# Kernel optimization log

Hardware: AMD Instinct MI355X
Metric: run time of the kernel (lower is better)

## Reference

```python
import jax, jax.numpy as jnp
import numpy as np

NUM_ATOMS = 1024
NUM_FEATS = 80      # c
NUM_IRREPS = 48     # (l_max+1)^2 * 3 with l_max=3
K3, K2, K1 = 1270, 24, 3  # CG-basis param counts per correlation order


def setup_inputs() -> dict:
    key = jax.random.key(0)
    ks = jax.random.split(key, 7)
    return {
        "node_feats": jax.random.normal(ks[0], (NUM_ATOMS, NUM_FEATS, NUM_IRREPS), jnp.float32),
        "U3": jax.random.normal(ks[1], (NUM_IRREPS, NUM_IRREPS, NUM_IRREPS, K3), jnp.float32),
        "U2": jax.random.normal(ks[2], (NUM_IRREPS, NUM_IRREPS, K2), jnp.float32),
        "U1": jax.random.normal(ks[3], (NUM_IRREPS, K1), jnp.float32),
        "W3": jax.random.normal(ks[4], (K3, NUM_FEATS), jnp.float32),
        "W2": jax.random.normal(ks[5], (K2, NUM_FEATS), jnp.float32),
        "W1": jax.random.normal(ks[6], (K1, NUM_FEATS), jnp.float32),
    }


def reference(node_feats, U3, U2, U1, W3, W2, W1):
    # equation_main: '...ik,kc,bci -> bc...' with U3 [p,q,i,k]
    # -> out [n, c, p, q]
    out = jnp.einsum('pqik,kc,nci->ncpq', U3, W3, node_feats)

    # corr = 2: c_tensor = einsum('...k,kc->c...', U2, W2) -> [c, p, q]
    c2 = jnp.einsum('pqk,kc->cpq', U2, W2) + out          # [n, c, p, q]
    # equation_contract: 'bc...i,bci->bc...'
    out = jnp.einsum('ncpi,nci->ncp', c2, node_feats)     # [n, c, p]

    # corr = 1: c_tensor = einsum('...k,kc->c...', U1, W1) -> [c, p]
    c1 = jnp.einsum('pk,kc->cp', U1, W1) + out            # [n, c, p]
    out = jnp.einsum('nci,nci->nc', c1, node_feats)       # [n, c]
    return out
```

## Files before the change

kernel.cpp:

```cpp
#include <hip/hip_runtime.h>
#include <hip/hip_bf16.h>

#define NA 1024
#define NC 80
#define NI 48
#define PQ (NI*NI)
#define M3 (PQ*NI)
#define K3 1270
#define K3P 1280
#define K2 24
#define K1 3

typedef __attribute__((ext_vector_type(8))) short bf16x8;
typedef __attribute__((ext_vector_type(4))) float f32x4;
typedef __attribute__((ext_vector_type(4))) unsigned int u32x4;

union BFPack { bf16x8 v; __hip_bfloat162 h[4]; };
union BF4 { uint2 u; __hip_bfloat162 h[2]; };
union BF2 { unsigned int u; __hip_bfloat162 h; };

__device__ __forceinline__ bf16x8 pack8(float a, float b, float c, float d,
                                        float e, float f, float g, float h) {
    BFPack u;
    u.h[0] = __float22bfloat162_rn(float2{a, b});
    u.h[1] = __float22bfloat162_rn(float2{c, d});
    u.h[2] = __float22bfloat162_rn(float2{e, f});
    u.h[3] = __float22bfloat162_rn(float2{g, h});
    return u.v;
}

__global__ __launch_bounds__(256) void k_w3t(const float* __restrict__ W3,
                                             __hip_bfloat16* __restrict__ W3bt) {
    int c = blockIdx.x;
    for (int k = threadIdx.x; k < K3P; k += 256) {
        float v = (k < K3) ? W3[(size_t)k * NC + c] : 0.f;
        W3bt[(size_t)c * K3P + k] = __float2bfloat16(v);
    }
}

__global__ __launch_bounds__(256) void k_uw3(const float* __restrict__ U3,
                                             const __hip_bfloat16* __restrict__ W3bt,
                                             __hip_bfloat16* __restrict__ UW3tb) {
    __shared__ __align__(16) unsigned short As[64 * 128];
    __shared__ __align__(16) unsigned short Bs[80 * 128];

    const int t    = threadIdx.x;
    const int wave = t >> 6;
    const int lane = t & 63;
    const int col  = lane & 15;
    const int quad = lane >> 4;

    const int m_base = blockIdx.x * 64;

    const float* __restrict__ aw = U3 + (size_t)(m_base + 16 * wave) * K3 + 2 * lane;
    char* asw = (char*)As + (16 * wave) * 256 + (lane & 3) * 4;
    const int ag = lane >> 2;

    f32x4 acc[5];
#pragma unroll
    for (int j = 0; j < 5; ++j) acc[j] = (f32x4)(0.f);

    float2 preA[16];
    u32x4  preB[5];

#pragma unroll
    for (int s = 0; s < 16; ++s)
        preA[s] = *(const float2*)(aw + (size_t)s * K3);
#pragma unroll
    for (int u = 0; u < 5; ++u) {
        int G = t + 256 * u, c = G >> 4, g = G & 15;
        preB[u] = *(const u32x4*)(W3bt + (size_t)c * K3P + g * 8);
    }

    for (int tile = 0; tile < 10; ++tile) {
        __syncthreads();
#pragma unroll
        for (int s = 0; s < 16; ++s) {
            BF2 w; w.h = __float22bfloat162_rn(preA[s]);
            *(unsigned int*)(asw + s * 256 + ((ag ^ (s & 7)) * 16)) = w.u;
        }
#pragma unroll
        for (int u = 0; u < 5; ++u) {
            int G = t + 256 * u, c = G >> 4, g = G & 15;
            *(u32x4*)((char*)Bs + c * 256 + ((g ^ (c & 7)) * 16)) = preB[u];
        }
        __syncthreads();

        if (tile < 9) {
            const int k0 = (tile + 1) * 128;
            const float* an = aw + k0;
            if (tile + 1 == 9) {
#pragma unroll
                for (int s = 0; s < 16; ++s)
                    preA[s] = (lane < 59) ? *(const float2*)(an + (size_t)s * K3)
                                          : float2{0.f, 0.f};
            } else {
#pragma unroll
                for (int s = 0; s < 16; ++s)
                    preA[s] = *(const float2*)(an + (size_t)s * K3);
            }
#pragma unroll
            for (int u = 0; u < 5; ++u) {
                int G = t + 256 * u, c = G >> 4, g = G & 15;
                preB[u] = *(const u32x4*)(W3bt + (size_t)c * K3P + k0 + g * 8);
            }
        }

        const int rbase = (16 * wave + col) * 256;
#pragma unroll
        for (int ks = 0; ks < 4; ++ks) {
            const int go = ((ks * 4 + quad) ^ (col & 7)) * 16;
            bf16x8 af = *(const bf16x8*)((const char*)As + rbase + go);
#pragma unroll
            for (int j = 0; j < 5; ++j) {
                bf16x8 bf = *(const bf16x8*)((const char*)Bs + (16 * j + col) * 256 + go);
                acc[j] = __builtin_amdgcn_mfma_f32_16x16x32_bf16(af, bf, acc[j], 0, 0, 0);
            }
        }
    }

#pragma unroll
    for (int j = 0; j < 5; ++j) {
        int c = 16 * j + col;
        size_t o = (size_t)c * M3 + m_base + 16 * wave + quad * 4;
        BF4 pk;
        pk.h[0] = __float22bfloat162_rn(float2{acc[j].x, acc[j].y});
        pk.h[1] = __float22bfloat162_rn(float2{acc[j].z, acc[j].w});
        *(uint2*)&UW3tb[o] = pk.u;
    }
}

__global__ __launch_bounds__(256) void k_c2t(const float* __restrict__ U2,
                                             const float* __restrict__ W2,
                                             float* __restrict__ c2t) {
    int idx = blockIdx.x * 256 + threadIdx.x;
    if (idx >= NC * PQ) return;
    int c  = idx / PQ;
    int pq = idx - c * PQ;
    float s = 0.f;
#pragma unroll
    for (int k = 0; k < K2; ++k) s += U2[pq * K2 + k] * W2[k * NC + c];
    c2t[idx] = s;
}

__global__ __launch_bounds__(256) void k_main(const float* __restrict__ nf,
                                              const __hip_bfloat16* __restrict__ UW3tb,
                                              const float* __restrict__ c2t,
                                              const float* __restrict__ U1,
                                              const float* __restrict__ W1,
                                              float* __restrict__ out) {
    __shared__ __align__(16) float Vs[64 * 52];
    __shared__ __align__(16) union { unsigned short vb[64 * 64];
                                     float red[64 * 17]; } VbRed;
    __shared__ __align__(16) unsigned short Ts[64 * 64];
    __shared__ __align__(16) float c2s[64];
    __shared__ __align__(16) float c1s[NI];

    const int t    = threadIdx.x;
    const int wave = t >> 6;
    const int col  = t & 15;
    const int quad = (t >> 4) & 3;

    const int bid = blockIdx.x;
    const int xcd = bid & 7;
    const int kb_ = bid >> 3;
    const int c   = xcd + 8 * (kb_ >> 4);
    const int nb  = kb_ & 15;
    const int n0  = nb * 64;

#pragma unroll
    for (int u = 0; u < 3; ++u) {
        int f   = t + 256 * u;
        int row = f / 12;
        int seg = f - row * 12;
        float4 v = *(const float4*)&nf[((size_t)(n0 + row) * NC + c) * NI + seg * 4];
        *(float4*)&Vs[row * 52 + seg * 4] = v;
        BF4 pk;
        pk.h[0] = __float22bfloat162_rn(float2{v.x, v.y});
        pk.h[1] = __float22bfloat162_rn(float2{v.z, v.w});
        *(uint2*)((char*)VbRed.vb + row * 128 + ((seg * 8) ^ ((row & 7) << 4))) = pk.u;
    }
    if (t < 128) {
        int row = t >> 1;
        int off = ((6 + (t & 1)) * 16) ^ ((row & 7) << 4);
        u32x4 z = (u32x4)(0u);
        *(u32x4*)((char*)VbRed.vb + row * 128 + off) = z;
        *(u32x4*)((char*)Ts       + row * 128 + off) = z;
    }
    if (t < NI) {
        float s = 0.f;
#pragma unroll
        for (int k = 0; k < K1; ++k) s += U1[t * K1 + k] * W1[k * NC + c];
        c1s[t] = s;
    }

    const __hip_bfloat16* Tcb = UW3tb + (size_t)c * M3;
    u32x4 pre0, pre1;
    pre0 = *(const u32x4*)(Tcb + (size_t)t * 8);
    if (t < 128) pre1 = *(const u32x4*)(Tcb + (size_t)(t + 256) * 8);

    __syncthreads();

    bf16x8 bfr[2][4];
#pragma unroll
    for (int s = 0; s < 2; ++s)
#pragma unroll
        for (int g = 0; g < 4; ++g) {
            int rw = 16 * g + col;
            bfr[s][g] = *(const bf16x8*)((const char*)VbRed.vb + rw * 128 +
                                         ((s * 64 + quad * 16) ^ ((rw & 7) << 4)));
        }
    int n52[4];
#pragma unroll
    for (int g = 0; g < 4; ++g) n52[g] = (16 * g + col) * 52;

    const int arow  = 16 * wave + col;
    const int abase = arow * 128;
    const int aswz  = (arow & 7) << 4;
    const int wq16  = 16 * wave + quad * 4;

    float oacc[4] = {0.f, 0.f, 0.f, 0.f};

    for (int tile = 0; tile < PQ / 64; ++tile) {
        __syncthreads();
        {
            int row = t / 6, seg = t - row * 6;
            *(u32x4*)((char*)Ts + row * 128 + ((seg * 16) ^ ((row & 7) << 4))) = pre0;
            if (t < 128) {
                int f2 = t + 256;
                int row2 = f2 / 6, seg2 = f2 - row2 * 6;
                *(u32x4*)((char*)Ts + row2 * 128 + ((seg2 * 16) ^ ((row2 & 7) << 4))) = pre1;
            }
        }
        if (t < 64) c2s[t] = c2t[(size_t)c * PQ + tile * 64 + t];
        __syncthreads();

        {
            int nt = (tile + 1 < PQ / 64) ? tile + 1 : tile;
            const __hip_bfloat16* src = Tcb + (size_t)nt * (64 * NI);
            pre0 = *(const u32x4*)(src + (size_t)t * 8);
            if (t < 128) pre1 = *(const u32x4*)(src + (size_t)(t + 256) * 8);
        }

        f32x4 acc[4];
#pragma unroll
        for (int g = 0; g < 4; ++g) acc[g] = (f32x4)(0.f);
#pragma unroll
        for (int s = 0; s < 2; ++s) {
            bf16x8 af = *(const bf16x8*)((const char*)Ts + abase +
                                         ((s * 64 + quad * 16) ^ aswz));
#pragma unroll
            for (int g = 0; g < 4; ++g)
                acc[g] = __builtin_amdgcn_mfma_f32_16x16x32_bf16(af, bfr[s][g], acc[g], 0, 0, 0);
        }

        int pqb = tile * 64 + wq16;
        int p   = (pqb * 21846) >> 20;
        int q0  = pqb - p * 48;
        f32x4 cv = *(const f32x4*)&c2s[wq16];
#pragma unroll
        for (int g = 0; g < 4; ++g) {
            float vp = Vs[n52[g] + p];
            f32x4 vq = *(const f32x4*)&Vs[n52[g] + q0];
#pragma unroll
            for (int r = 0; r < 4; ++r)
                oacc[g] += (acc[g][r] + cv[r]) * vp * vq[r];
        }
    }

    __syncthreads();
#pragma unroll
    for (int g = 0; g < 4; ++g)
        VbRed.red[(16 * g + col) * 17 + (t >> 4)] = oacc[g];
    __syncthreads();
    if (t < 64) {
        float s = 0.f;
#pragma unroll
        for (int j = 0; j < 16; ++j) s += VbRed.red[t * 17 + j];
#pragma unroll
        for (int p = 0; p < NI; ++p) s += c1s[p] * Vs[t * 52 + p];
        out[(size_t)(n0 + t) * NC + c] = s;
    }
}

extern "C" void kernel_launch(void* const* d_in, const int* in_sizes, int n_in,
                              void* d_out, int out_size, void* d_ws, size_t ws_size,
                              hipStream_t stream) {
    const float* nf = (const float*)d_in[0];
    const float* U3 = (const float*)d_in[1];
    const float* U2 = (const float*)d_in[2];
    const float* U1 = (const float*)d_in[3];
    const float* W3 = (const float*)d_in[4];
    const float* W2 = (const float*)d_in[5];
    const float* W1 = (const float*)d_in[6];
    float* out = (float*)d_out;

    __hip_bfloat16* UW3tb = (__hip_bfloat16*)d_ws;
    float* c2tw = (float*)((char*)d_ws + (size_t)NC * M3 * 2);
    __hip_bfloat16* W3bt = (__hip_bfloat16*)c2tw;

    k_w3t <<<NC,                    256, 0, stream>>>(W3, W3bt);
    k_uw3 <<<M3 / 64,               256, 0, stream>>>(U3, W3bt, UW3tb);
    k_c2t <<<(NC * PQ + 255) / 256, 256, 0, stream>>>(U2, W2, c2tw);
    k_main<<<NC * 16,               256, 0, stream>>>(nf, UW3tb, c2tw, U1, W1, out);
}
```

Baseline: 810.6 us.

## Double-buffer U3 prefetch in k_uw3 and merge prep kernels into one launch

Merges the W3 transpose and the c2 tensor computation into a single prep kernel, which removes one launch, and gives W3bt its own workspace region so it no longer aliases c2t. In the U3·W3 GEMM kernel, the A operand is now prefetched two tiles ahead using two register buffers, while B is prefetched one tile ahead. The goal is to hide the global-load latency of the large U3 stream behind MFMA compute. The cost is higher register pressure from the extra 16 float2 buffer, which could lower occupancy.

```diff
diff --git a/kernel.cpp b/kernel.cpp
--- a/kernel.cpp
+++ b/kernel.cpp
@@ -29,12 +29,27 @@
     return u.v;
 }
 
-__global__ __launch_bounds__(256) void k_w3t(const float* __restrict__ W3,
-                                             __hip_bfloat16* __restrict__ W3bt) {
-    int c = blockIdx.x;
-    for (int k = threadIdx.x; k < K3P; k += 256) {
-        float v = (k < K3) ? W3[(size_t)k * NC + c] : 0.f;
-        W3bt[(size_t)c * K3P + k] = __float2bfloat16(v);
+__global__ __launch_bounds__(256) void k_prep(const float* __restrict__ W3,
+                                              const float* __restrict__ U2,
+                                              const float* __restrict__ W2,
+                                              __hip_bfloat16* __restrict__ W3bt,
+                                              float* __restrict__ c2t) {
+    int b = blockIdx.x;
+    if (b < NC) {
+        int c = b;
+        for (int k = threadIdx.x; k < K3P; k += 256) {
+            float v = (k < K3) ? W3[(size_t)k * NC + c] : 0.f;
+            W3bt[(size_t)c * K3P + k] = __float2bfloat16(v);
+        }
+    } else {
+        int idx = (b - NC) * 256 + threadIdx.x;
+        if (idx >= NC * PQ) return;
+        int c  = idx / PQ;
+        int pq = idx - c * PQ;
+        float s = 0.f;
+#pragma unroll
+        for (int k = 0; k < K2; ++k) s += U2[pq * K2 + k] * W2[k * NC + c];
+        c2t[idx] = s;
     }
 }
 
@@ -60,52 +75,45 @@
 #pragma unroll
     for (int j = 0; j < 5; ++j) acc[j] = (f32x4)(0.f);
 
-    float2 preA[16];
-    u32x4  preB[5];
-
-#pragma unroll
-    for (int s = 0; s < 16; ++s)
-        preA[s] = *(const float2*)(aw + (size_t)s * K3);
-#pragma unroll
-    for (int u = 0; u < 5; ++u) {
-        int G = t + 256 * u, c = G >> 4, g = G & 15;
-        preB[u] = *(const u32x4*)(W3bt + (size_t)c * K3P + g * 8);
-    }
-
-    for (int tile = 0; tile < 10; ++tile) {
-        __syncthreads();
-#pragma unroll
-        for (int s = 0; s < 16; ++s) {
-            BF2 w; w.h = __float22bfloat162_rn(preA[s]);
-            *(unsigned int*)(asw + s * 256 + ((ag ^ (s & 7)) * 16)) = w.u;
-        }
+    float2 pA0[16], pA1[16];
+    u32x4  pB[5];
+
+    auto loadA = [&](float2* dst, int tl) {
+        const float* an = aw + tl * 128;
+        if (tl == 9) {
+#pragma unroll
+            for (int s = 0; s < 16; ++s)
+                dst[s] = (lane < 59) ? *(const float2*)(an + (size_t)s * K3)
+                                     : float2{0.f, 0.f};
+        } else {
+#pragma unroll
+            for (int s = 0; s < 16; ++s)
+                dst[s] = *(const float2*)(an + (size_t)s * K3);
+        }
+    };
+    auto loadB = [&](int tl) {
+        const int k0 = tl * 128;
 #pragma unroll
         for (int u = 0; u < 5; ++u) {
             int G = t + 256 * u, c = G >> 4, g = G & 15;
-            *(u32x4*)((char*)Bs + c * 256 + ((g ^ (c & 7)) * 16)) = preB[u];
-        }
-        __syncthreads();
-
-        if (tile < 9) {
-            const int k0 = (tile + 1) * 128;
-            const float* an = aw + k0;
-            if (tile + 1 == 9) {
-#pragma unroll
-                for (int s = 0; s < 16; ++s)
-                    preA[s] = (lane < 59) ? *(const float2*)(an + (size_t)s * K3)
-                                          : float2{0.f, 0.f};
-            } else {
-#pragma unroll
-                for (int s = 0; s < 16; ++s)
-                    preA[s] = *(const float2*)(an + (size_t)s * K3);
-            }
-#pragma unroll
-            for (int u = 0; u < 5; ++u) {
-                int G = t + 256 * u, c = G >> 4, g = G & 15;
-                preB[u] = *(const u32x4*)(W3bt + (size_t)c * K3P + k0 + g * 8);
-            }
-        }
-
+            pB[u] = *(const u32x4*)(W3bt + (size_t)c * K3P + k0 + g * 8);
+        }
+    };
+    auto writeA = [&](const float2* src) {
+#pragma unroll
+        for (int s = 0; s < 16; ++s) {
+            BF2 w; w.h = __float22bfloat162_rn(src[s]);
+            *(unsigned int*)(asw + s * 256 + ((ag ^ (s & 7)) * 16)) = w.u;
+        }
+    };
+    auto writeB = [&]() {
+#pragma unroll
+        for (int u = 0; u < 5; ++u) {
+            int G = t + 256 * u, c = G >> 4, g = G & 15;
+            *(u32x4*)((char*)Bs + c * 256 + ((g ^ (c & 7)) * 16)) = pB[u];
+        }
+    };
+    auto compute = [&]() {
         const int rbase = (16 * wave + col) * 256;
 #pragma unroll
         for (int ks = 0; ks < 4; ++ks) {
@@ -117,6 +125,32 @@
                 acc[j] = __builtin_amdgcn_mfma_f32_16x16x32_bf16(af, bf, acc[j], 0, 0, 0);
             }
         }
+    };
+
+    loadA(pA0, 0);
+    loadB(0);
+    loadA(pA1, 1);
+
+#pragma unroll 1
+    for (int t2 = 0; t2 < 5; ++t2) {
+        const int tileA = 2 * t2;
+        const int tileB = 2 * t2 + 1;
+
+        __syncthreads();
+        writeA(pA0);
+        writeB();
+        __syncthreads();
+        if (tileA + 2 <= 9) loadA(pA0, tileA + 2);
+        loadB(tileB);
+        compute();
+
+        __syncthreads();
+        writeA(pA1);
+        writeB();
+        __syncthreads();
+        if (tileB + 2 <= 9) loadA(pA1, tileB + 2);
+        if (tileB + 1 <= 9) loadB(tileB + 1);
+        compute();
     }
 
 #pragma unroll
@@ -128,19 +162,6 @@
         pk.h[1] = __float22bfloat162_rn(float2{acc[j].z, acc[j].w});
         *(uint2*)&UW3tb[o] = pk.u;
     }
-}
-
-__global__ __launch_bounds__(256) void k_c2t(const float* __restrict__ U2,
-                                             const float* __restrict__ W2,
-                                             float* __restrict__ c2t) {
-    int idx = blockIdx.x * 256 + threadIdx.x;
-    if (idx >= NC * PQ) return;
-    int c  = idx / PQ;
-    int pq = idx - c * PQ;
-    float s = 0.f;
-#pragma unroll
-    for (int k = 0; k < K2; ++k) s += U2[pq * K2 + k] * W2[k * NC + c];
-    c2t[idx] = s;
 }
 
 __global__ __launch_bounds__(256) void k_main(const float* __restrict__ nf,
@@ -297,10 +318,10 @@
 
     __hip_bfloat16* UW3tb = (__hip_bfloat16*)d_ws;
     float* c2tw = (float*)((char*)d_ws + (size_t)NC * M3 * 2);
-    __hip_bfloat16* W3bt = (__hip_bfloat16*)c2tw;
-
-    k_w3t <<<NC,                    256, 0, stream>>>(W3, W3bt);
-    k_uw3 <<<M3 / 64,               256, 0, stream>>>(U3, W3bt, UW3tb);
-    k_c2t <<<(NC * PQ + 255) / 256, 256, 0, stream>>>(U2, W2, c2tw);
-    k_main<<<NC * 16,               256, 0, stream>>>(nf, UW3tb, c2tw, U1, W1, out);
-}
+    __hip_bfloat16* W3bt = (__hip_bfloat16*)((char*)d_ws +
+                           (size_t)NC * M3 * 2 + (size_t)NC * PQ * 4);
+
+    k_prep<<<NC + (NC * PQ + 255) / 256, 256, 0, stream>>>(W3, U2, W2, W3bt, c2tw);
+    k_uw3 <<<M3 / 64,                    256, 0, stream>>>(U3, W3bt, UW3tb);
+    k_main<<<NC * 16,                    256, 0, stream>>>(nf, UW3tb, c2tw, U1, W1, out);
+}
```

After: 817.8 us. No clear change (+0.9%).
